# Optimization experiments

Hardware: AMD Instinct MI355X
Metric: run time of the kernel (lower is better)

The kernel has to match this reference:

```python
import jax, jax.numpy as jnp
import numpy as np

ALPHA = 0.1      # GNN-LF teleport/restart coefficient
K_ITERS = 4      # high-order: 4 propagation iterates, concatenated -> BN width = 4*output_dim
BN_EPS = 1e-5

B, N, DIN, DOUT = 2, 8192, 64, 32


def setup_inputs() -> dict:
    key = jax.random.key(0)
    ks = jax.random.split(key, 5)
    x = jax.random.normal(ks[0], (B, N, DIN), dtype=jnp.float32)
    x0 = jax.random.normal(ks[1], (B, N, DIN), dtype=jnp.float32)
    # random sparse-ish row-normalized adjacency (dense buffer, as in the module)
    a = jax.random.uniform(ks[2], (N, N), dtype=jnp.float32)
    a = jnp.where(a > 0.995, a, 0.0)
    a = a + jnp.eye(N, dtype=jnp.float32)  # self loops
    adj = a / jnp.sum(a, axis=1, keepdims=True)
    W = jax.random.normal(ks[3], (DIN, DOUT), dtype=jnp.float32) / np.sqrt(DIN)
    W0 = jax.random.normal(ks[4], (DIN, DOUT), dtype=jnp.float32) / np.sqrt(DIN)
    gamma = jnp.ones((K_ITERS * DOUT,), dtype=jnp.float32)
    beta = jnp.zeros((K_ITERS * DOUT,), dtype=jnp.float32)
    return {"x": x, "x0": x0, "adj": adj, "W": W, "W0": W0, "gamma": gamma, "beta": beta}


def _gnn_lf(x, x0, adj, W, W0):
    # linear projections
    h = jnp.einsum("bnd,df->bnf", x, W)      # [B,N,DOUT]
    h0 = jnp.einsum("bnd,df->bnf", x0, W0)   # [B,N,DOUT]
    hk = h
    outs = []
    for _ in range(K_ITERS):  # fixed small unroll over propagation order
        hk = (1.0 - ALPHA) * jnp.einsum("nm,bmf->bnf", adj, hk) + ALPHA * h0
        outs.append(hk)
    return jnp.concatenate(outs, axis=-1)    # [B,N,4*DOUT]


def reference(x, x0, adj, W, W0, gamma, beta):
    y = _gnn_lf(x, x0, adj, W, W0)                      # [B,N,C], C=4*DOUT
    # transpose(1,2) -> BatchNorm1d over channel C (stats over B and N) -> transpose back
    mean = jnp.mean(y, axis=(0, 1))                     # [C]
    var = jnp.var(y, axis=(0, 1))                       # [C] (biased, as torch BN training)
    y = (y - mean) * jax.lax.rsqrt(var + BN_EPS) * gamma + beta
    # p_dropout is None -> single ReLU
    return jax.nn.relu(y)
```

## Files before the change

kernel.cpp:

```cpp
#include <hip/hip_runtime.h>
#include <hip/hip_bf16.h>
#include <stdint.h>


#define NN 8192
#define CAP 128

typedef __hip_bfloat16 bf16;
typedef unsigned short ushort_t;

__device__ __forceinline__ float b2f_bits(unsigned short u) {
    union { unsigned int i; float f; } c;
    c.i = ((unsigned int)u) << 16;
    return c.f;
}

__global__ void k_sniff(const unsigned int* __restrict__ g, int* __restrict__ flag) {
    *flag = (g[0] == 0x3F803F80u) ? 1 : 0;
}

__global__ __launch_bounds__(256) void k_proj(const void* __restrict__ xv,
                                              const void* __restrict__ x0v,
                                              const void* __restrict__ Wv,
                                              const void* __restrict__ W0v,
                                              const int* __restrict__ flag,
                                              float* __restrict__ Hh,
                                              float* __restrict__ H0) {
    __shared__ float Ws[64][32];
    __shared__ float W0s[64][32];
    __shared__ float xs[4][2][64];
    __shared__ float x0s[4][2][64];
    int t = threadIdx.x;
    int n0 = blockIdx.x * 4;
    int isbf = *flag;
    if (isbf) {
        const ushort_t* W  = (const ushort_t*)Wv;
        const ushort_t* W0 = (const ushort_t*)W0v;
        const ushort_t* x  = (const ushort_t*)xv;
        const ushort_t* x0 = (const ushort_t*)x0v;
#pragma unroll
        for (int i = 0; i < 8; ++i) {
            int idx = t + i * 256;
            Ws[idx >> 5][idx & 31]  = b2f_bits(W[idx]);
            W0s[idx >> 5][idx & 31] = b2f_bits(W0[idx]);
        }
#pragma unroll
        for (int i = 0; i < 2; ++i) {
            int idx = t + i * 256;
            int r = idx >> 7, b = (idx >> 6) & 1, d = idx & 63;
            size_t g = ((size_t)(b * NN + n0 + r)) * 64 + d;
            xs[r][b][d]  = b2f_bits(x[g]);
            x0s[r][b][d] = b2f_bits(x0[g]);
        }
    } else {
        const float* W  = (const float*)Wv;
        const float* W0 = (const float*)W0v;
        const float* x  = (const float*)xv;
        const float* x0 = (const float*)x0v;
#pragma unroll
        for (int i = 0; i < 8; ++i) {
            int idx = t + i * 256;
            Ws[idx >> 5][idx & 31]  = W[idx];
            W0s[idx >> 5][idx & 31] = W0[idx];
        }
#pragma unroll
        for (int i = 0; i < 2; ++i) {
            int idx = t + i * 256;
            int r = idx >> 7, b = (idx >> 6) & 1, d = idx & 63;
            size_t g = ((size_t)(b * NN + n0 + r)) * 64 + d;
            xs[r][b][d]  = x[g];
            x0s[r][b][d] = x0[g];
        }
    }
    __syncthreads();
    int c2 = t & 63, r = t >> 6;
    int b = c2 >> 5, f = c2 & 31;
    float a = 0.f, a0 = 0.f;
#pragma unroll
    for (int d = 0; d < 64; ++d) {
        a  += xs[r][b][d]  * Ws[d][f];
        a0 += x0s[r][b][d] * W0s[d][f];
    }
    int o = (n0 + r) * 64 + c2;
    Hh[o] = a;
    H0[o] = a0;
}

__global__ __launch_bounds__(256) void k_build(const void* __restrict__ adjv,
                                               const int* __restrict__ flag,
                                               int* __restrict__ nnz,
                                               int* __restrict__ ellcol,
                                               float* __restrict__ ellval) {
    int w = threadIdx.x >> 6, lane = threadIdx.x & 63;
    int row = blockIdx.x * 4 + w;
    __shared__ int cnt[4];
    if (lane == 0) cnt[w] = 0;
    __syncthreads();
    int*   crow = ellcol + row * CAP;
    float* vrow = ellval + row * CAP;
    int isbf = *flag;
    if (isbf) {
        const uint4* rp = (const uint4*)((const ushort_t*)adjv + (size_t)row * NN);
        for (int chunk = 0; chunk < 16; ++chunk) {
            uint4 v = rp[chunk * 64 + lane];
            int cb = chunk * 512 + lane * 8;
            unsigned int words[4] = {v.x, v.y, v.z, v.w};
#pragma unroll
            for (int q = 0; q < 4; ++q) {
                unsigned int u = words[q];
                unsigned short lo = (unsigned short)(u & 0xffffu);
                unsigned short hi = (unsigned short)(u >> 16);
                if (lo) {
                    int s = atomicAdd(&cnt[w], 1);
                    if (s < CAP) { crow[s] = cb + 2 * q;     vrow[s] = b2f_bits(lo); }
                }
                if (hi) {
                    int s = atomicAdd(&cnt[w], 1);
                    if (s < CAP) { crow[s] = cb + 2 * q + 1; vrow[s] = b2f_bits(hi); }
                }
            }
        }
    } else {
        const float4* rp = (const float4*)((const float*)adjv + (size_t)row * NN);
        for (int chunk = 0; chunk < 32; ++chunk) {
            float4 v = rp[chunk * 64 + lane];
            int cb = chunk * 256 + lane * 4;
            float vals[4] = {v.x, v.y, v.z, v.w};
#pragma unroll
            for (int q = 0; q < 4; ++q) {
                if (vals[q] != 0.f) {
                    int s = atomicAdd(&cnt[w], 1);
                    if (s < CAP) { crow[s] = cb + q; vrow[s] = vals[q]; }
                }
            }
        }
    }
    __syncthreads();
    if (lane == 0) nnz[row] = cnt[w] < CAP ? cnt[w] : CAP;
}

__global__ __launch_bounds__(256) void k_spmm(const int* __restrict__ nnz,
                                              const int* __restrict__ ellcol,
                                              const float* __restrict__ ellval,
                                              const float* __restrict__ Hprev,
                                              const float* __restrict__ H0,
                                              float* __restrict__ Hnext) {
    int w = threadIdx.x >> 6, lane = threadIdx.x & 63;
    int row = blockIdx.x * 4 + w;
    int cnt = nnz[row];
    const int*   cr = ellcol + row * CAP;
    const float* vr = ellval + row * CAP;
    float acc = 0.f;
    int j = 0;
    for (; j + 4 <= cnt; j += 4) {
        int   c0 = cr[j], c1 = cr[j + 1], c2 = cr[j + 2], c3 = cr[j + 3];
        float v0 = vr[j], v1 = vr[j + 1], v2 = vr[j + 2], v3 = vr[j + 3];
        acc += v0 * Hprev[c0 * 64 + lane];
        acc += v1 * Hprev[c1 * 64 + lane];
        acc += v2 * Hprev[c2 * 64 + lane];
        acc += v3 * Hprev[c3 * 64 + lane];
    }
    for (; j < cnt; ++j) acc += vr[j] * Hprev[cr[j] * 64 + lane];
    int o = row * 64 + lane;
    Hnext[o] = 0.9f * acc + 0.1f * H0[o];
}

__global__ __launch_bounds__(256) void k_stats1(const float* __restrict__ Hk0,
                                                const float* __restrict__ Hk1,
                                                const float* __restrict__ Hk2,
                                                const float* __restrict__ Hk3,
                                                float* __restrict__ partial) {
    const float* Hs[4] = {Hk0, Hk1, Hk2, Hk3};
    int c2 = threadIdx.x & 63, rg = threadIdx.x >> 6;
    int rb = blockIdx.x * 128;
    float s[4] = {0, 0, 0, 0}, q[4] = {0, 0, 0, 0};
    for (int r = rb + rg; r < rb + 128; r += 4) {
#pragma unroll
        for (int k = 0; k < 4; ++k) {
            float v = Hs[k][r * 64 + c2];
            s[k] += v;
            q[k] += v * v;
        }
    }
    __shared__ float red[4][64];
#pragma unroll
    for (int k = 0; k < 4; ++k) {
        red[rg][c2] = s[k];
        __syncthreads();
        if (rg == 0)
            partial[((blockIdx.x * 4 + k) * 64 + c2) * 2 + 0] =
                red[0][c2] + red[1][c2] + red[2][c2] + red[3][c2];
        __syncthreads();
        red[rg][c2] = q[k];
        __syncthreads();
        if (rg == 0)
            partial[((blockIdx.x * 4 + k) * 64 + c2) * 2 + 1] =
                red[0][c2] + red[1][c2] + red[2][c2] + red[3][c2];
        __syncthreads();
    }
}

__global__ void k_stats2(const float* __restrict__ partial,
                         const void* __restrict__ gv,
                         const void* __restrict__ bv,
                         const int* __restrict__ flag,
                         float* __restrict__ ss) {
    int c = threadIdx.x;
    if (c >= 128) return;
    int k = c >> 5, f = c & 31;
    float s = 0.f, q = 0.f;
    for (int blk = 0; blk < 64; ++blk) {
        int b0 = ((blk * 4 + k) * 64 + f) * 2;
        int b1 = ((blk * 4 + k) * 64 + 32 + f) * 2;
        s += partial[b0] + partial[b1];
        q += partial[b0 + 1] + partial[b1 + 1];
    }
    float mean = s * (1.f / 16384.f);
    float var  = q * (1.f / 16384.f) - mean * mean;
    float gm, bt;
    if (*flag) {
        gm = b2f_bits(((const ushort_t*)gv)[c]);
        bt = b2f_bits(((const ushort_t*)bv)[c]);
    } else {
        gm = ((const float*)gv)[c];
        bt = ((const float*)bv)[c];
    }
    float sc = gm * rsqrtf(var + 1e-5f);
    ss[c] = sc;
    ss[128 + c] = bt - mean * sc;
}

__global__ __launch_bounds__(256) void k_out(const float* __restrict__ Hk0,
                                             const float* __restrict__ Hk1,
                                             const float* __restrict__ Hk2,
                                             const float* __restrict__ Hk3,
                                             const float* __restrict__ ss,
                                             const int* __restrict__ flag,
                                             void* __restrict__ out) {
    int idx = blockIdx.x * 256 + threadIdx.x;
    int c = idx & 127;
    int n_b = idx >> 7;
    int b = n_b >> 13;
    int n = n_b & 8191;
    int k = c >> 5, f = c & 31;
    const float* H = (k == 0) ? Hk0 : (k == 1) ? Hk1 : (k == 2) ? Hk2 : Hk3;
    float v = H[n * 64 + b * 32 + f];
    float o = v * ss[c] + ss[128 + c];
    o = fmaxf(o, 0.f);
    if (*flag) ((bf16*)out)[idx] = __float2bfloat16(o);
    else       ((float*)out)[idx] = o;
}

extern "C" void kernel_launch(void* const* d_in, const int* in_sizes, int n_in,
                              void* d_out, int out_size, void* d_ws, size_t ws_size,
                              hipStream_t stream) {
    const void* x     = d_in[0];
    const void* x0    = d_in[1];
    const void* adj   = d_in[2];
    const void* W     = d_in[3];
    const void* W0    = d_in[4];
    const void* gamma = d_in[5];
    const void* beta  = d_in[6];

    float* fw     = (float*)d_ws;
    float* Hh     = fw;
    float* H0     = Hh + NN * 64;
    float* Hk0    = H0  + NN * 64;
    float* Hk1    = Hk0 + NN * 64;
    float* Hk2    = Hk1 + NN * 64;
    float* Hk3    = Hk2 + NN * 64;
    float* ellval = Hk3 + NN * 64;
    float* part   = ellval + NN * CAP;
    float* ss     = part + 64 * 4 * 64 * 2;
    int*   ellcol = (int*)(ss + 256);
    int*   nnz    = ellcol + NN * CAP;
    int*   flag   = nnz + NN;

    k_sniff<<<1, 1, 0, stream>>>((const unsigned int*)gamma, flag);
    k_proj <<<NN / 4, 256, 0, stream>>>(x, x0, W, W0, flag, Hh, H0);
    k_build<<<NN / 4, 256, 0, stream>>>(adj, flag, nnz, ellcol, ellval);
    k_spmm <<<NN / 4, 256, 0, stream>>>(nnz, ellcol, ellval, Hh,  H0, Hk0);
    k_spmm <<<NN / 4, 256, 0, stream>>>(nnz, ellcol, ellval, Hk0, H0, Hk1);
    k_spmm <<<NN / 4, 256, 0, stream>>>(nnz, ellcol, ellval, Hk1, H0, Hk2);
    k_spmm <<<NN / 4, 256, 0, stream>>>(nnz, ellcol, ellval, Hk2, H0, Hk3);
    k_stats1<<<64, 256, 0, stream>>>(Hk0, Hk1, Hk2, Hk3, part);
    k_stats2<<<1, 128, 0, stream>>>(part, gamma, beta, flag, ss);
    k_out  <<<(2 * NN * 128) / 256, 256, 0, stream>>>(Hk0, Hk1, Hk2, Hk3, ss, flag, d_out);
}
```

Measured before the change: 458.4 us.

## Tile projection, shuffle-broadcast ELL indices in spmm, vectorize output writes

The projection kernel now has each block handle 32 rows with register tiling and padded shared memory, instead of 4 rows with one output per thread. The SpMM kernel loads each row's column indices and values once per lane and broadcasts them with wave shuffles, with rows padded to a multiple of 8 by writing zero entries. The output kernel reads and writes four channels per thread using float4 or ushort4 accesses. The main cost is still the dense adjacency scan in k_build, so these changes only touch the smaller stages.

```diff
diff --git a/kernel.cpp b/kernel.cpp
--- a/kernel.cpp
+++ b/kernel.cpp
@@ -13,6 +13,10 @@
     union { unsigned int i; float f; } c;
     c.i = ((unsigned int)u) << 16;
     return c.f;
+}
+__device__ __forceinline__ unsigned short f2b_bits(float f) {
+    bf16 h = __float2bfloat16(f);
+    return *(unsigned short*)&h;
 }
 
 __global__ void k_sniff(const unsigned int* __restrict__ g, int* __restrict__ flag) {
@@ -26,12 +30,12 @@
                                               const int* __restrict__ flag,
                                               float* __restrict__ Hh,
                                               float* __restrict__ H0) {
-    __shared__ float Ws[64][32];
-    __shared__ float W0s[64][32];
-    __shared__ float xs[4][2][64];
-    __shared__ float x0s[4][2][64];
+    __shared__ float X[64][65];
+    __shared__ float X0[64][65];
+    __shared__ float Ws[64][33];
+    __shared__ float W0s[64][33];
     int t = threadIdx.x;
-    int n0 = blockIdx.x * 4;
+    int n0 = blockIdx.x * 32;
     int isbf = *flag;
     if (isbf) {
         const ushort_t* W  = (const ushort_t*)Wv;
@@ -45,12 +49,12 @@
             W0s[idx >> 5][idx & 31] = b2f_bits(W0[idx]);
         }
 #pragma unroll
-        for (int i = 0; i < 2; ++i) {
+        for (int i = 0; i < 16; ++i) {
             int idx = t + i * 256;
-            int r = idx >> 7, b = (idx >> 6) & 1, d = idx & 63;
+            int d = idx & 63, l = idx >> 6, b = l >> 5, r = l & 31;
             size_t g = ((size_t)(b * NN + n0 + r)) * 64 + d;
-            xs[r][b][d]  = b2f_bits(x[g]);
-            x0s[r][b][d] = b2f_bits(x0[g]);
+            X[l][d]  = b2f_bits(x[g]);
+            X0[l][d] = b2f_bits(x0[g]);
         }
     } else {
         const float* W  = (const float*)Wv;
@@ -64,26 +68,44 @@
             W0s[idx >> 5][idx & 31] = W0[idx];
         }
 #pragma unroll
-        for (int i = 0; i < 2; ++i) {
+        for (int i = 0; i < 16; ++i) {
             int idx = t + i * 256;
-            int r = idx >> 7, b = (idx >> 6) & 1, d = idx & 63;
+            int d = idx & 63, l = idx >> 6, b = l >> 5, r = l & 31;
             size_t g = ((size_t)(b * NN + n0 + r)) * 64 + d;
-            xs[r][b][d]  = x[g];
-            x0s[r][b][d] = x0[g];
+            X[l][d]  = x[g];
+            X0[l][d] = x0[g];
         }
     }
     __syncthreads();
-    int c2 = t & 63, r = t >> 6;
-    int b = c2 >> 5, f = c2 & 31;
-    float a = 0.f, a0 = 0.f;
-#pragma unroll
+    int c2g = t & 15, rg = t >> 4;
+    float aA[2][4] = {{0,0,0,0},{0,0,0,0}};
+    float aB[2][4] = {{0,0,0,0},{0,0,0,0}};
+#pragma unroll 4
     for (int d = 0; d < 64; ++d) {
-        a  += xs[r][b][d]  * Ws[d][f];
-        a0 += x0s[r][b][d] * W0s[d][f];
-    }
-    int o = (n0 + r) * 64 + c2;
-    Hh[o] = a;
-    H0[o] = a0;
+        float w0 = Ws[d][c2g],  w1 = Ws[d][c2g + 16];
+        float u0 = W0s[d][c2g], u1 = W0s[d][c2g + 16];
+#pragma unroll
+        for (int p = 0; p < 2; ++p) {
+            float xa = X[rg + 16 * p][d];
+            float xb = X[32 + rg + 16 * p][d];
+            float ya = X0[rg + 16 * p][d];
+            float yb = X0[32 + rg + 16 * p][d];
+            aA[p][0] += xa * w0; aA[p][1] += xa * w1;
+            aA[p][2] += xb * w0; aA[p][3] += xb * w1;
+            aB[p][0] += ya * u0; aB[p][1] += ya * u1;
+            aB[p][2] += yb * u0; aB[p][3] += yb * u1;
+        }
+    }
+#pragma unroll
+    for (int p = 0; p < 2; ++p) {
+        int row = n0 + rg + 16 * p;
+#pragma unroll
+        for (int q = 0; q < 4; ++q) {
+            int c2 = c2g + 16 * q;
+            Hh[row * 64 + c2] = aA[p][q];
+            H0[row * 64 + c2] = aB[p][q];
+        }
+    }
 }
 
 __global__ __launch_bounds__(256) void k_build(const void* __restrict__ adjv,
@@ -136,7 +158,12 @@
         }
     }
     __syncthreads();
-    if (lane == 0) nnz[row] = cnt[w] < CAP ? cnt[w] : CAP;
+    int c = cnt[w];
+    if (c > CAP) c = CAP;
+    int padded = (c + 7) & ~7;
+    if (padded > CAP) padded = CAP;
+    for (int s = c + lane; s < padded; s += 64) { crow[s] = 0; vrow[s] = 0.f; }
+    if (lane == 0) nnz[row] = padded;
 }
 
 __global__ __launch_bounds__(256) void k_spmm(const int* __restrict__ nnz,
@@ -150,17 +177,27 @@
     int cnt = nnz[row];
     const int*   cr = ellcol + row * CAP;
     const float* vr = ellval + row * CAP;
+    int   myc = cr[lane];
+    float myv = vr[lane];
     float acc = 0.f;
-    int j = 0;
-    for (; j + 4 <= cnt; j += 4) {
-        int   c0 = cr[j], c1 = cr[j + 1], c2 = cr[j + 2], c3 = cr[j + 3];
-        float v0 = vr[j], v1 = vr[j + 1], v2 = vr[j + 2], v3 = vr[j + 3];
-        acc += v0 * Hprev[c0 * 64 + lane];
-        acc += v1 * Hprev[c1 * 64 + lane];
-        acc += v2 * Hprev[c2 * 64 + lane];
-        acc += v3 * Hprev[c3 * 64 + lane];
-    }
-    for (; j < cnt; ++j) acc += vr[j] * Hprev[cr[j] * 64 + lane];
+    int m = cnt < 64 ? cnt : 64;
+#pragma unroll 8
+    for (int j = 0; j < m; ++j) {
+        int   c = __shfl(myc, j);
+        float v = __shfl(myv, j);
+        acc += v * Hprev[c * 64 + lane];
+    }
+    if (cnt > 64) {
+        int   myc2 = cr[64 + lane];
+        float myv2 = vr[64 + lane];
+        int m2 = cnt - 64;
+#pragma unroll 8
+        for (int j = 0; j < m2; ++j) {
+            int   c = __shfl(myc2, j);
+            float v = __shfl(myv2, j);
+            acc += v * Hprev[c * 64 + lane];
+        }
+    }
     int o = row * 64 + lane;
     Hnext[o] = 0.9f * acc + 0.1f * H0[o];
 }
@@ -237,18 +274,26 @@
                                              const float* __restrict__ ss,
                                              const int* __restrict__ flag,
                                              void* __restrict__ out) {
-    int idx = blockIdx.x * 256 + threadIdx.x;
-    int c = idx & 127;
-    int n_b = idx >> 7;
-    int b = n_b >> 13;
-    int n = n_b & 8191;
-    int k = c >> 5, f = c & 31;
+    int q = blockIdx.x * 256 + threadIdx.x;
+    int c0 = (q & 31) * 4;
+    int nb = q >> 5;
+    int b = nb >> 13, n = nb & 8191;
+    int k = c0 >> 5, f = c0 & 31;
     const float* H = (k == 0) ? Hk0 : (k == 1) ? Hk1 : (k == 2) ? Hk2 : Hk3;
-    float v = H[n * 64 + b * 32 + f];
-    float o = v * ss[c] + ss[128 + c];
-    o = fmaxf(o, 0.f);
-    if (*flag) ((bf16*)out)[idx] = __float2bfloat16(o);
-    else       ((float*)out)[idx] = o;
+    float4 v  = *(const float4*)(H + n * 64 + b * 32 + f);
+    float4 sc = *(const float4*)(ss + c0);
+    float4 sh = *(const float4*)(ss + 128 + c0);
+    float o0 = fmaxf(v.x * sc.x + sh.x, 0.f);
+    float o1 = fmaxf(v.y * sc.y + sh.y, 0.f);
+    float o2 = fmaxf(v.z * sc.z + sh.z, 0.f);
+    float o3 = fmaxf(v.w * sc.w + sh.w, 0.f);
+    if (*flag) {
+        ushort4 u;
+        u.x = f2b_bits(o0); u.y = f2b_bits(o1); u.z = f2b_bits(o2); u.w = f2b_bits(o3);
+        *(ushort4*)((ushort_t*)out + (size_t)q * 4) = u;
+    } else {
+        *(float4*)((float*)out + (size_t)q * 4) = make_float4(o0, o1, o2, o3);
+    }
 }
 
 extern "C" void kernel_launch(void* const* d_in, const int* in_sizes, int n_in,
@@ -277,7 +322,7 @@
     int*   flag   = nnz + NN;
 
     k_sniff<<<1, 1, 0, stream>>>((const unsigned int*)gamma, flag);
-    k_proj <<<NN / 4, 256, 0, stream>>>(x, x0, W, W0, flag, Hh, H0);
+    k_proj <<<NN / 32, 256, 0, stream>>>(x, x0, W, W0, flag, Hh, H0);
     k_build<<<NN / 4, 256, 0, stream>>>(adj, flag, nnz, ellcol, ellval);
     k_spmm <<<NN / 4, 256, 0, stream>>>(nnz, ellcol, ellval, Hh,  H0, Hk0);
     k_spmm <<<NN / 4, 256, 0, stream>>>(nnz, ellcol, ellval, Hk0, H0, Hk1);
@@ -285,5 +330,5 @@
     k_spmm <<<NN / 4, 256, 0, stream>>>(nnz, ellcol, ellval, Hk2, H0, Hk3);
     k_stats1<<<64, 256, 0, stream>>>(Hk0, Hk1, Hk2, Hk3, part);
     k_stats2<<<1, 128, 0, stream>>>(part, gamma, beta, flag, ss);
-    k_out  <<<(2 * NN * 128) / 256, 256, 0, stream>>>(Hk0, Hk1, Hk2, Hk3, ss, flag, d_out);
-}
+    k_out  <<<2 * NN * 32 / 256, 256, 0, stream>>>(Hk0, Hk1, Hk2, Hk3, ss, flag, d_out);
+}
```

Measured after the change: 485.9 us. +6.0%, slower.
